# Kernel tuning notes

Hardware: AMD Instinct MI355X
Metric: run time of the kernel (lower is better)

## Reference

```python
import jax, jax.numpy as jnp
import numpy as np


def conv1x1(x, w, b):
    # x: [B,C,H,W], w: [O,C], b: [O]
    return jnp.einsum('bchw,oc->bohw', x, w) + b[None, :, None, None]


def dwconv(x, w):
    # depthwise conv, x: [B,C,H,W], w: [C,1,k,k], SAME padding (k odd, pad=k//2)
    return jax.lax.conv_general_dilated(
        x, w, window_strides=(1, 1), padding='SAME',
        dimension_numbers=('NCHW', 'OIHW', 'NCHW'),
        feature_group_count=x.shape[1])


def setup_inputs() -> dict:
    key = jax.random.key(0)
    ks = jax.random.split(key, 14)
    B, C, H, W = 16, 256, 64, 64
    OC = C // 16  # scale=16 -> 16
    WSCALE = 0.05
    r = lambda k, shape: jax.random.normal(k, shape, dtype=jnp.float32) * WSCALE
    return {
        'x': jax.random.normal(ks[0], (B, C, H, W), dtype=jnp.float32),
        'conv_w': r(ks[1], (C + 4, C)),           # 1x1 conv -> ctx (C) + gates (3+1)
        'conv_b': r(ks[2], (C + 4,)),
        'fw3': r(ks[3], (C, 1, 3, 3)),            # depthwise focal kernels
        'fw5': r(ks[4], (C, 1, 5, 5)),
        'fw7': r(ks[5], (C, 1, 7, 7)),
        'key_w': r(ks[6], (1, C)),                # Conv_key 1x1
        'key_b': r(ks[7], (1,)),
        'v1_w': r(ks[8], (OC, C)),                # Conv_value first 1x1
        'v1_b': r(ks[9], (OC,)),
        'ln_w': jnp.ones((OC,), dtype=jnp.float32),
        'ln_b': jnp.zeros((OC,), dtype=jnp.float32),
        'v2_w': r(ks[10], (C, OC)),               # Conv_value second 1x1
        'v2_b': r(ks[11], (C,)),
    }


def reference(x, conv_w, conv_b, fw3, fw5, fw7, key_w, key_b,
              v1_w, v1_b, ln_w, ln_b, v2_w, v2_b):
    B, C, H, W = x.shape
    # _contextAggregation
    t = conv1x1(x, conv_w, conv_b)          # [B, C+4, H, W]
    ctx, gates = t[:, :C], t[:, C:]         # [B,C,H,W], [B,4,H,W]
    ctx_all = jnp.zeros_like(ctx)
    for l, fw in enumerate((fw3, fw5, fw7)):
        ctx = jax.nn.gelu(dwconv(ctx, fw), approximate=False)  # torch GELU = exact erf
        ctx_all = ctx_all + ctx * gates[:, l:l + 1]
    ctx_global = jnp.mean(ctx, axis=(2, 3), keepdims=True)     # AdaptiveAvgPool2d(1)
    ctx_all = ctx_all + ctx_global * gates[:, 3:4]
    # GC-style channel attention: softmax over spatial positions
    k = conv1x1(ctx_all, key_w, key_b).reshape(B, H * W)       # [B, HW]
    k = jax.nn.softmax(k, axis=1)
    q = ctx_all.reshape(B, C, H * W)
    qk = jnp.einsum('bcn,bn->bc', q, k)[:, :, None, None]      # [B,C,1,1]
    # Conv_value: 1x1 -> LayerNorm([OC,1,1]) -> ReLU -> 1x1
    v = conv1x1(qk, v1_w, v1_b)                                # [B,OC,1,1]
    mu = jnp.mean(v, axis=(1, 2, 3), keepdims=True)
    var = jnp.var(v, axis=(1, 2, 3), keepdims=True)
    v = (v - mu) * jax.lax.rsqrt(var + 1e-5)
    v = v * ln_w[None, :, None, None] + ln_b[None, :, None, None]
    v = jax.nn.relu(v)
    v = conv1x1(v, v2_w, v2_b)                                 # [B,C,1,1]
    return ctx_all + v
```

## Files before the change

kernel.cpp:

```cpp
#include <hip/hip_runtime.h>

#define DEVFN __device__ __forceinline__

constexpr int B  = 16;
constexpr int C  = 256;
constexpr int N  = 64 * 64;
constexpr int O1 = C + 4;

typedef __attribute__((ext_vector_type(8)))  short bf16x8;
typedef __attribute__((ext_vector_type(4)))  short bf16x4;
typedef __attribute__((ext_vector_type(16))) float f32x16;
typedef __attribute__((ext_vector_type(2)))  _Float16 h2;
typedef unsigned short ushort_t;
typedef unsigned int   uint32;

DEVFN short f2bf(float f){
  union { float f; unsigned u; } p; p.f = f;
  unsigned r = p.u + 0x7fffu + ((p.u >> 16) & 1u);
  return (short)(r >> 16);
}
DEVFN unsigned pack2(float lo, float hi){
  return (unsigned)(ushort_t)f2bf(lo) | ((unsigned)(ushort_t)f2bf(hi) << 16);
}
DEVFN float lo2f(unsigned u){ union{unsigned u; float f;} p; p.u = u << 16; return p.f; }
DEVFN float hi2f(unsigned u){ union{unsigned u; float f;} p; p.u = u & 0xffff0000u; return p.f; }
DEVFN float bf2f(ushort_t s){ union{unsigned u; float f;} p; p.u = (unsigned)s << 16; return p.f; }

DEVFN float gelu_fast(float x){
  float s = x * x;
  float t = x * fmaf(s, 0.1029432f, 2.3022082f);
  float e = __builtin_amdgcn_exp2f(-t);
  return x * __builtin_amdgcn_rcpf(1.0f + e);
}

DEVFN float fdot2f(uint32 a, uint32 b, float c){
#if __has_builtin(__builtin_amdgcn_fdot2)
  return __builtin_amdgcn_fdot2(__builtin_bit_cast(h2, a),
                                __builtin_bit_cast(h2, b), c, false);
#else
  h2 ha = __builtin_bit_cast(h2, a), hb = __builtin_bit_cast(h2, b);
  return fmaf((float)ha.x, (float)hb.x, fmaf((float)ha.y, (float)hb.y, c));
#endif
}

DEVFN uint32 pkh(float a, float b){
  _Float16 ha = (_Float16)a, hb = (_Float16)b;
  return (uint32)__builtin_bit_cast(ushort_t, ha) |
         ((uint32)__builtin_bit_cast(ushort_t, hb) << 16);
}

__global__ __launch_bounds__(256)
void k_wbf(const float* __restrict__ w, ushort_t* __restrict__ wbf,
           const float* __restrict__ fw3, const float* __restrict__ fw5,
           const float* __restrict__ fw7, uint32* __restrict__ w3p,
           uint32* __restrict__ w5p, uint32* __restrict__ w7p,
           const float* __restrict__ x, ushort_t* __restrict__ xbf){
  if(blockIdx.x >= 321){
    const int blk = blockIdx.x - 321;
    const int b  = blk >> 5;
    const int kg = blk & 31;
    const float* xs = x + ((size_t)(b * 256 + kg * 8)) * N;
    ushort_t* xd = xbf + ((size_t)(b * 32 + kg)) * N * 8;
    #pragma unroll
    for(int it = 0; it < 4; it++){
      const int n = (it * 256 + threadIdx.x) * 4;
      float4 cv[8];
      #pragma unroll
      for(int j = 0; j < 8; j++) cv[j] = *(const float4*)(xs + (size_t)j * N + n);
      #pragma unroll
      for(int p = 0; p < 4; p++){
        uint4 v;
        v.x = pack2(((const float*)&cv[0])[p], ((const float*)&cv[1])[p]);
        v.y = pack2(((const float*)&cv[2])[p], ((const float*)&cv[3])[p]);
        v.z = pack2(((const float*)&cv[4])[p], ((const float*)&cv[5])[p]);
        v.w = pack2(((const float*)&cv[6])[p], ((const float*)&cv[7])[p]);
        *(uint4*)(xd + (size_t)(n + p) * 8) = v;
      }
    }
    return;
  }
  if(blockIdx.x == 320){
    const int c = threadIdx.x;
    #pragma unroll
    for(int ky = 0; ky < 3; ky++){
      const float* wr = fw3 + c * 9 + ky * 3;
      w3p[c * 6 + ky * 2 + 0] = pkh(wr[0], wr[1]);
      w3p[c * 6 + ky * 2 + 1] = pkh(wr[2], 0.f);
    }
    #pragma unroll
    for(int ky = 0; ky < 5; ky++){
      const float* wr = fw5 + c * 25 + ky * 5;
      w5p[c * 15 + ky * 3 + 0] = pkh(wr[0], wr[1]);
      w5p[c * 15 + ky * 3 + 1] = pkh(wr[2], wr[3]);
      w5p[c * 15 + ky * 3 + 2] = pkh(wr[4], 0.f);
    }
    #pragma unroll
    for(int ky = 0; ky < 7; ky++){
      const float* wr = fw7 + c * 49 + ky * 7;
      w7p[c * 28 + ky * 4 + 0] = pkh(wr[0], wr[1]);
      w7p[c * 28 + ky * 4 + 1] = pkh(wr[2], wr[3]);
      w7p[c * 28 + ky * 4 + 2] = pkh(wr[4], wr[5]);
      w7p[c * 28 + ky * 4 + 3] = pkh(wr[6], 0.f);
    }
    return;
  }
  int idx = blockIdx.x * 256 + threadIdx.x;
  int o = idx >> 8, cc = idx & 255;
  wbf[idx] = (o < O1) ? (ushort_t)f2bf(w[o * 256 + cc]) : (ushort_t)0;
}

__global__ __launch_bounds__(512, 6)
void k_conv1_mfma(const ushort_t* __restrict__ xbf, const ushort_t* __restrict__ wbf,
                  const float* __restrict__ conv_w, const float* __restrict__ bias,
                  ushort_t* __restrict__ ctxb, float* __restrict__ gates){
  __shared__ __align__(16) short wlds[8 * 256 * 8];
  __shared__ __align__(16) short xlds[2][8 * 64 * 8];
  __shared__ float sgw[4 * 256];
  __shared__ float sbias[256];
  const int tid  = threadIdx.x;
  const int wave = tid >> 6;
  const int lane = tid & 63;
  const int l31  = lane & 31;
  const int lhi  = lane >> 5;
  const int pg   = blockIdx.x;
  const int b    = pg >> 6;
  const int n0   = (pg & 63) * 64;

  #pragma unroll
  for(int i = 0; i < 2; i++) sgw[i * 512 + tid] = conv_w[256 * 256 + i * 512 + tid];
  if(tid < 256) sbias[tid] = bias[tid];
  const int gidx = tid >> 6;
  const int gn   = tid & 63;
  float gbias = (tid < 256) ? bias[256 + gidx] : 0.f;
  float gacc = 0.f;

  f32x16 acc[2];
  #pragma unroll
  for(int t = 0; t < 2; t++)
    #pragma unroll
    for(int r = 0; r < 16; r++) acc[t][r] = 0.f;

  auto glX = [&](int kc, int bf){
    const ushort_t* src = xbf + ((size_t)(b * 32 + (kc >> 3) + wave) * N + n0 + lane) * 8;
    __builtin_amdgcn_global_load_lds(
        (const __attribute__((address_space(1))) unsigned int*)src,
        (__attribute__((address_space(3))) unsigned int*)&xlds[bf][(size_t)tid * 8],
        16, 0, 0);
  };
  auto glW = [&](int kc){
    #pragma unroll
    for(int q = 0; q < 4; q++){
      const int pidx = q * 512 + tid;
      const int kg = pidx >> 8;
      const int m  = pidx & 255;
      const ushort_t* src = wbf + (size_t)m * 256 + kc + kg * 8;
      __builtin_amdgcn_global_load_lds(
          (const __attribute__((address_space(1))) unsigned int*)src,
          (__attribute__((address_space(3))) unsigned int*)&wlds[(size_t)pidx * 8],
          16, 0, 0);
    }
  };
  auto mfmaC = [&](const short* xb){
    #pragma unroll
    for(int ks = 0; ks < 4; ks++){
      const int kg = ks * 2 + lhi;
      bf16x8 af = *(const bf16x8*)&wlds[(kg * 256 + wave * 32 + l31) * 8];
      bf16x8 b0 = *(const bf16x8*)&xb[(kg * 64 + l31) * 8];
      bf16x8 b1 = *(const bf16x8*)&xb[(kg * 64 + 32 + l31) * 8];
      acc[0] = __builtin_amdgcn_mfma_f32_32x32x16_bf16(af, b0, acc[0], 0, 0, 0);
      acc[1] = __builtin_amdgcn_mfma_f32_32x32x16_bf16(af, b1, acc[1], 0, 0, 0);
    }
  };
  auto gateC = [&](const short* xb, int kc){
    if(tid < 256){
      float a = gacc;
      #pragma unroll
      for(int kg = 0; kg < 8; kg++){
        bf16x8 xv = *(const bf16x8*)&xb[(kg * 64 + gn) * 8];
        const float* gw = &sgw[gidx * 256 + kc + kg * 8];
        #pragma unroll
        for(int j = 0; j < 4; j++){
          unsigned u = ((const unsigned*)&xv)[j];
          a = fmaf(lo2f(u), gw[2 * j], a);
          a = fmaf(hi2f(u), gw[2 * j + 1], a);
        }
      }
      gacc = a;
    }
  };

  glX(0, 0); glW(0);
  __syncthreads();
  glX(64, 1);
  mfmaC(xlds[0]); gateC(xlds[0], 0);
  __syncthreads();
  glW(64);
  __syncthreads();
  glX(128, 0);
  mfmaC(xlds[1]); gateC(xlds[1], 64);
  __syncthreads();
  glW(128);
  __syncthreads();
  glX(192, 1);
  mfmaC(xlds[0]); gateC(xlds[0], 128);
  __syncthreads();
  glW(192);
  __syncthreads();
  mfmaC(xlds[1]); gateC(xlds[1], 192);

  #pragma unroll
  for(int nt = 0; nt < 2; nt++){
    const int n = n0 + nt * 32 + l31;
    #pragma unroll
    for(int r = 0; r < 16; r++){
      const int row = (r & 3) + 8 * (r >> 2) + 4 * lhi;
      const int o = wave * 32 + row;
      const float v = acc[nt][r] + sbias[o];
      _Float16 hv = (_Float16)v;
      ctxb[((size_t)(b * 256 + o)) * N + n] = __builtin_bit_cast(ushort_t, hv);
    }
  }
  if(tid < 256)
    gates[((size_t)(b * 4 + gidx)) * N + n0 + gn] = gacc + gbias;
}

constexpr int SSTR = 72;

template<int K>
DEVFN void dw_stage_dot(const short* src, const uint32* __restrict__ wp,
                        int h, int w0, float* val){
  constexpr int R = K / 2;
  constexpr int PAIRS = (K + 2) / 2;
  float acc[8];
  #pragma unroll
  for(int i = 0; i < 8; i++) acc[i] = 0.f;
  #pragma unroll
  for(int ky = 0; ky < K; ky++){
    uint32 wk[PAIRS];
    #pragma unroll
    for(int t = 0; t < PAIRS; t++) wk[t] = wp[ky * PAIRS + t];
    const int r = h + ky - R;
    if((unsigned)r < 64u){
      const short* rp = &src[r * SSTR + w0];
      uint4 a0 = *(const uint4*)rp;
      uint4 a1 = *(const uint4*)(rp + 8);
      uint32 P[8] = {a0.x, a0.y, a0.z, a0.w, a1.x, a1.y, a1.z, a1.w};
      uint32 S[7];
      #pragma unroll
      for(int j = 0; j < 7; j++)
        S[j] = __builtin_amdgcn_alignbit(P[j + 1], P[j], 16);
      #pragma unroll
      for(int i = 0; i < 8; i++){
        int j0, useP;
        if      (K == 7){ useP =  (i & 1); j0 = (i + 1) >> 1; }
        else if (K == 5){ useP = !(i & 1); j0 = (i >> 1) + 1; }
        else            { useP =  (i & 1); j0 = (i >> 1) + ((i & 1) ? 2 : 1); }
        #pragma unroll
        for(int t = 0; t < PAIRS; t++){
          const uint32 a = useP ? P[j0 + t] : S[j0 + t];
          acc[i] = fdot2f(a, wk[t], acc[i]);
        }
      }
    }
  }
  #pragma unroll
  for(int i = 0; i < 8; i++) val[i] = gelu_fast(acc[i]);
}

DEVFN void store_row_h(short* dst, int h, int w0, const float* val){
  uint32 o0 = __builtin_bit_cast(uint32, __builtin_amdgcn_cvt_pkrtz(val[0], val[1]));
  uint32 o1 = __builtin_bit_cast(uint32, __builtin_amdgcn_cvt_pkrtz(val[2], val[3]));
  uint32 o2 = __builtin_bit_cast(uint32, __builtin_amdgcn_cvt_pkrtz(val[4], val[5]));
  uint32 o3 = __builtin_bit_cast(uint32, __builtin_amdgcn_cvt_pkrtz(val[6], val[7]));
  uint2 t0; t0.x = o0; t0.y = o1;
  uint2 t1; t1.x = o2; t1.y = o3;
  *(uint2*)&dst[h * SSTR + w0 + 4] = t0;
  *(uint2*)&dst[h * SSTR + w0 + 8] = t1;
}

__global__ __launch_bounds__(512, 8)
void k_dwchain(ushort_t* __restrict__ ctxb, const uint32* __restrict__ w3p,
               const uint32* __restrict__ w5p, const uint32* __restrict__ w7p,
               const float* __restrict__ gates){
  __shared__ __align__(16) short bufA[64 * SSTR];
  __shared__ __align__(16) short bufB[64 * SSTR];
  __shared__ float wred[8];
  const int tid = threadIdx.x;
  const int plane = blockIdx.x;
  const int b = plane >> 8;
  const int c = plane & 255;
  const int h  = tid >> 3;
  const int w0 = (tid & 7) * 8;
  const int nbase = h * 64 + w0;

  if(tid < 64){
    bf16x4 z = {0, 0, 0, 0};
    *(bf16x4*)&bufA[tid * SSTR] = z;  *(bf16x4*)&bufA[tid * SSTR + 68] = z;
    *(bf16x4*)&bufB[tid * SSTR] = z;  *(bf16x4*)&bufB[tid * SSTR + 68] = z;
  }
  {
    const uint4 iv = *(const uint4*)((const short*)ctxb + (size_t)plane * N + tid * 8);
    uint2 t0; t0.x = iv.x; t0.y = iv.y;
    uint2 t1; t1.x = iv.z; t1.y = iv.w;
    *(uint2*)&bufA[h * SSTR + w0 + 4] = t0;
    *(uint2*)&bufA[h * SSTR + w0 + 8] = t1;
  }
  __syncthreads();

  float ctxp[8];
  #pragma unroll
  for(int i = 0; i < 8; i++) ctxp[i] = 0.f;
  float val[8];

  dw_stage_dot<3>(bufA, w3p + c * 6, h, w0, val);
  {
    const float* gp = gates + ((size_t)(b * 4 + 0)) * N + nbase;
    float4 ga = *(const float4*)gp, gb = *(const float4*)(gp + 4);
    ctxp[0] = fmaf(val[0], ga.x, ctxp[0]); ctxp[1] = fmaf(val[1], ga.y, ctxp[1]);
    ctxp[2] = fmaf(val[2], ga.z, ctxp[2]); ctxp[3] = fmaf(val[3], ga.w, ctxp[3]);
    ctxp[4] = fmaf(val[4], gb.x, ctxp[4]); ctxp[5] = fmaf(val[5], gb.y, ctxp[5]);
    ctxp[6] = fmaf(val[6], gb.z, ctxp[6]); ctxp[7] = fmaf(val[7], gb.w, ctxp[7]);
    store_row_h(bufB, h, w0, val);
  }
  __syncthreads();

  dw_stage_dot<5>(bufB, w5p + c * 15, h, w0, val);
  {
    const float* gp = gates + ((size_t)(b * 4 + 1)) * N + nbase;
    float4 ga = *(const float4*)gp, gb = *(const float4*)(gp + 4);
    ctxp[0] = fmaf(val[0], ga.x, ctxp[0]); ctxp[1] = fmaf(val[1], ga.y, ctxp[1]);
    ctxp[2] = fmaf(val[2], ga.z, ctxp[2]); ctxp[3] = fmaf(val[3], ga.w, ctxp[3]);
    ctxp[4] = fmaf(val[4], gb.x, ctxp[4]); ctxp[5] = fmaf(val[5], gb.y, ctxp[5]);
    ctxp[6] = fmaf(val[6], gb.z, ctxp[6]); ctxp[7] = fmaf(val[7], gb.w, ctxp[7]);
    store_row_h(bufA, h, w0, val);
  }
  __syncthreads();

  dw_stage_dot<7>(bufA, w7p + c * 28, h, w0, val);
  float lsum = 0.f;
  {
    const float* gp = gates + ((size_t)(b * 4 + 2)) * N + nbase;
    float4 ga = *(const float4*)gp, gb = *(const float4*)(gp + 4);
    ctxp[0] = fmaf(val[0], ga.x, ctxp[0]); ctxp[1] = fmaf(val[1], ga.y, ctxp[1]);
    ctxp[2] = fmaf(val[2], ga.z, ctxp[2]); ctxp[3] = fmaf(val[3], ga.w, ctxp[3]);
    ctxp[4] = fmaf(val[4], gb.x, ctxp[4]); ctxp[5] = fmaf(val[5], gb.y, ctxp[5]);
    ctxp[6] = fmaf(val[6], gb.z, ctxp[6]); ctxp[7] = fmaf(val[7], gb.w, ctxp[7]);
    #pragma unroll
    for(int i = 0; i < 8; i++) lsum += val[i];
  }
  #pragma unroll
  for(int off = 32; off > 0; off >>= 1) lsum += __shfl_xor(lsum, off, 64);
  if((tid & 63) == 0) wred[tid >> 6] = lsum;
  __syncthreads();
  float mean = 0.f;
  #pragma unroll
  for(int i = 0; i < 8; i++) mean += wred[i];
  mean *= (1.0f / 4096.0f);

  {
    const float* gp = gates + ((size_t)(b * 4 + 3)) * N + nbase;
    float4 ga = *(const float4*)gp, gb = *(const float4*)(gp + 4);
    bf16x8 ov;
    ov[0] = f2bf(fmaf(mean, ga.x, ctxp[0])); ov[1] = f2bf(fmaf(mean, ga.y, ctxp[1]));
    ov[2] = f2bf(fmaf(mean, ga.z, ctxp[2])); ov[3] = f2bf(fmaf(mean, ga.w, ctxp[3]));
    ov[4] = f2bf(fmaf(mean, gb.x, ctxp[4])); ov[5] = f2bf(fmaf(mean, gb.y, ctxp[5]));
    ov[6] = f2bf(fmaf(mean, gb.z, ctxp[6])); ov[7] = f2bf(fmaf(mean, gb.w, ctxp[7]));
    *(bf16x8*)((short*)ctxb + (size_t)plane * N + nbase) = ov;
  }
}

__global__ __launch_bounds__(256)
void k_logits(const ushort_t* __restrict__ P, const float* __restrict__ key_w,
              const float* __restrict__ key_b, float* __restrict__ logits){
  __shared__ float kw[256];
  __shared__ float part[512];
  int tid = threadIdx.x;
  kw[tid] = key_w[tid];
  __syncthreads();
  int b  = blockIdx.x >> 5;
  int n0 = (blockIdx.x & 31) * 128;
  int cpart = tid >> 6, pxp = tid & 63;
  const ushort_t* pp = P + ((size_t)(b * 256 + cpart * 64)) * N + n0 + pxp * 2;
  float a0 = 0.f, a1 = 0.f;
  #pragma unroll 8
  for(int c = 0; c < 64; c++){
    unsigned u = *(const unsigned*)(pp + (size_t)c * N);
    float kwv = kw[cpart * 64 + c];
    a0 = fmaf(lo2f(u), kwv, a0);
    a1 = fmaf(hi2f(u), kwv, a1);
  }
  part[cpart * 128 + pxp * 2]     = a0;
  part[cpart * 128 + pxp * 2 + 1] = a1;
  __syncthreads();
  if(tid < 128){
    float l = part[tid] + part[128 + tid] + part[256 + tid] + part[384 + tid];
    logits[b * N + n0 + tid] = l + key_b[0];
  }
}

__global__ __launch_bounds__(1024)
void k_softmax(float* __restrict__ kbuf){
  __shared__ float wred[16];
  int b = blockIdx.x, tid = threadIdx.x;
  const int wave = tid >> 6, lane = tid & 63;
  float v[4];
  float m = -1e30f;
  #pragma unroll
  for(int i = 0; i < 4; i++){
    v[i] = kbuf[b * N + tid + i * 1024];
    m = fmaxf(m, v[i]);
  }
  #pragma unroll
  for(int off = 32; off > 0; off >>= 1) m = fmaxf(m, __shfl_xor(m, off, 64));
  if(lane == 0) wred[wave] = m;
  __syncthreads();
  float mm = -1e30f;
  #pragma unroll
  for(int i = 0; i < 16; i++) mm = fmaxf(mm, wred[i]);
  __syncthreads();
  float s = 0.f;
  #pragma unroll
  for(int i = 0; i < 4; i++){ v[i] = __expf(v[i] - mm); s += v[i]; }
  #pragma unroll
  for(int off = 32; off > 0; off >>= 1) s += __shfl_xor(s, off, 64);
  if(lane == 0) wred[wave] = s;
  __syncthreads();
  float tot = 0.f;
  #pragma unroll
  for(int i = 0; i < 16; i++) tot += wred[i];
  float inv = 1.0f / tot;
  #pragma unroll
  for(int i = 0; i < 4; i++)
    kbuf[b * N + tid + i * 1024] = v[i] * inv;
}

__global__ __launch_bounds__(256)
void k_qk(const ushort_t* __restrict__ P, const float* __restrict__ kbuf,
          float* __restrict__ qk){
  __shared__ float red[256];
  int plane = blockIdx.x, tid = threadIdx.x;
  int b = plane >> 8;
  const unsigned* pp = (const unsigned*)(P + (size_t)plane * N);
  const float2* kp = (const float2*)(kbuf + b * N);
  float acc = 0.f;
  #pragma unroll
  for(int i = 0; i < 8; i++){
    int idx = tid + i * 256;
    unsigned u = pp[idx];
    float2 kk = kp[idx];
    acc = fmaf(lo2f(u), kk.x, acc);
    acc = fmaf(hi2f(u), kk.y, acc);
  }
  red[tid] = acc; __syncthreads();
  for(int s = 128; s > 0; s >>= 1){
    if(tid < s) red[tid] += red[tid + s];
    __syncthreads();
  }
  if(tid == 0) qk[plane] = red[0];
}

__global__ __launch_bounds__(256)
void k_v(const float* __restrict__ qk, const float* __restrict__ v1w,
         const float* __restrict__ v1b, const float* __restrict__ lnw,
         const float* __restrict__ lnb, const float* __restrict__ v2w,
         const float* __restrict__ v2b, float* __restrict__ vout){
  int b = blockIdx.x, tid = threadIdx.x;
  __shared__ float qs[256];
  __shared__ float part[256];
  __shared__ float v1s[16];
  __shared__ float vr[16];
  __shared__ float stats[2];
  qs[tid] = qk[b * 256 + tid];
  __syncthreads();
  int oc = tid >> 4, ln = tid & 15;
  float p = 0.f;
  #pragma unroll
  for(int j = 0; j < 16; j++){
    int cc = ln + j * 16;
    p = fmaf(v1w[oc * 256 + cc], qs[cc], p);
  }
  part[tid] = p;
  __syncthreads();
  if(tid < 16){
    float s = v1b[tid];
    for(int j = 0; j < 16; j++) s += part[tid * 16 + j];
    v1s[tid] = s;
  }
  __syncthreads();
  if(tid == 0){
    float mu = 0.f;
    for(int i = 0; i < 16; i++) mu += v1s[i];
    mu *= (1.f / 16.f);
    float var = 0.f;
    for(int i = 0; i < 16; i++){ float d = v1s[i] - mu; var += d * d; }
    var *= (1.f / 16.f);
    stats[0] = mu; stats[1] = rsqrtf(var + 1e-5f);
  }
  __syncthreads();
  if(tid < 16){
    float vv = (v1s[tid] - stats[0]) * stats[1] * lnw[tid] + lnb[tid];
    vr[tid] = fmaxf(vv, 0.f);
  }
  __syncthreads();
  float o = v2b[tid];
  #pragma unroll
  for(int j = 0; j < 16; j++) o = fmaf(v2w[tid * 16 + j], vr[j], o);
  vout[b * 256 + tid] = o;
}

__global__ __launch_bounds__(256)
void k_final(float* __restrict__ out, const ushort_t* __restrict__ ctxb,
             const float* __restrict__ vout){
  int idx8 = blockIdx.x * 256 + threadIdx.x;
  int plane = idx8 >> 9;
  int off = (idx8 & 511) * 8;
  bf16x8 v = *(const bf16x8*)((const short*)ctxb + (size_t)plane * N + off);
  float vv = vout[plane];
  float4 o0, o1;
  o0.x = bf2f((ushort_t)v[0]) + vv; o0.y = bf2f((ushort_t)v[1]) + vv;
  o0.z = bf2f((ushort_t)v[2]) + vv; o0.w = bf2f((ushort_t)v[3]) + vv;
  o1.x = bf2f((ushort_t)v[4]) + vv; o1.y = bf2f((ushort_t)v[5]) + vv;
  o1.z = bf2f((ushort_t)v[6]) + vv; o1.w = bf2f((ushort_t)v[7]) + vv;
  float* op = out + (size_t)plane * N + off;
  *(float4*)op = o0;
  *(float4*)(op + 4) = o1;
}

extern "C" void kernel_launch(void* const* d_in, const int* in_sizes, int n_in,
                              void* d_out, int out_size, void* d_ws, size_t ws_size,
                              hipStream_t stream){
  const float* x      = (const float*)d_in[0];
  const float* conv_w = (const float*)d_in[1];
  const float* conv_b = (const float*)d_in[2];
  const float* fw3    = (const float*)d_in[3];
  const float* fw5    = (const float*)d_in[4];
  const float* fw7    = (const float*)d_in[5];
  const float* key_w  = (const float*)d_in[6];
  const float* key_b  = (const float*)d_in[7];
  const float* v1_w   = (const float*)d_in[8];
  const float* v1_b   = (const float*)d_in[9];
  const float* ln_w   = (const float*)d_in[10];
  const float* ln_b   = (const float*)d_in[11];
  const float* v2_w   = (const float*)d_in[12];
  const float* v2_b   = (const float*)d_in[13];
  float* out = (float*)d_out;

  const size_t PL = (size_t)B * C * N;
  char* p = (char*)d_ws;
  ushort_t* ctxb = (ushort_t*)p;  p += PL * sizeof(ushort_t);
  float* gates   = (float*)p;     p += (size_t)B * 4 * N * sizeof(float);
  float* kbuf    = (float*)p;     p += (size_t)B * N * sizeof(float);
  float* qkb     = (float*)p;     p += (size_t)B * C * sizeof(float);
  float* vout    = (float*)p;     p += (size_t)B * C * sizeof(float);
  ushort_t* wbf  = (ushort_t*)p;  p += (size_t)320 * 256 * sizeof(ushort_t);
  uint32* w3p    = (uint32*)p;    p += (size_t)256 * 6 * sizeof(uint32);
  uint32* w5p    = (uint32*)p;    p += (size_t)256 * 15 * sizeof(uint32);
  uint32* w7p    = (uint32*)p;
  ushort_t* xbf  = (ushort_t*)d_out;

  k_wbf<<<833, 256, 0, stream>>>(conv_w, wbf, fw3, fw5, fw7, w3p, w5p, w7p,
                                 x, xbf);
  k_conv1_mfma<<<1024, 512, 0, stream>>>(xbf, wbf, conv_w, conv_b, ctxb, gates);
  k_dwchain<<<B * C, 512, 0, stream>>>(ctxb, w3p, w5p, w7p, gates);
  k_logits<<<512, 256, 0, stream>>>(ctxb, key_w, key_b, kbuf);
  k_softmax<<<B, 1024, 0, stream>>>(kbuf);
  k_qk<<<B * C, 256, 0, stream>>>(ctxb, kbuf, qkb);
  k_v<<<B, 256, 0, stream>>>(qkb, v1_w, v1_b, ln_w, ln_b, v2_w, v2_b, vout);
  k_final<<<8192, 256, 0, stream>>>(out, ctxb, vout);
}
```

Measured before the change: 266.8 us.

## Fuse key-logit reduction into depthwise chain via global atomics

Removes the separate k_logits kernel, which re-read the whole bf16 ctx tensor. Each k_dwchain thread now atomically adds key_w[c] times its fp32 ctx_all values into a logits buffer, and k_wbf zeroes that buffer first. key_b is dropped because softmax is invariant to a constant shift. The trade-off is about 16M float atomics, with 256 channels contending for each pixel address, plus nondeterministic summation order. The dwchain occupancy hint also drops from 8 to 6 waves.

```diff
diff --git a/kernel.cpp b/kernel.cpp
--- a/kernel.cpp
+++ b/kernel.cpp
@@ -54,7 +54,8 @@
            const float* __restrict__ fw3, const float* __restrict__ fw5,
            const float* __restrict__ fw7, uint32* __restrict__ w3p,
            uint32* __restrict__ w5p, uint32* __restrict__ w7p,
-           const float* __restrict__ x, ushort_t* __restrict__ xbf){
+           const float* __restrict__ x, ushort_t* __restrict__ xbf,
+           float* __restrict__ kbuf){
   if(blockIdx.x >= 321){
     const int blk = blockIdx.x - 321;
     const int b  = blk >> 5;
@@ -101,6 +102,11 @@
       w7p[c * 28 + ky * 4 + 1] = pkh(wr[2], wr[3]);
       w7p[c * 28 + ky * 4 + 2] = pkh(wr[4], wr[5]);
       w7p[c * 28 + ky * 4 + 3] = pkh(wr[6], 0.f);
+    }
+    float4* kz = (float4*)kbuf;
+    for(int it = 0; it < 64; it++){
+      float4 z; z.x = 0.f; z.y = 0.f; z.z = 0.f; z.w = 0.f;
+      kz[it * 256 + threadIdx.x] = z;
     }
     return;
   }
@@ -278,10 +284,11 @@
   *(uint2*)&dst[h * SSTR + w0 + 8] = t1;
 }
 
-__global__ __launch_bounds__(512, 8)
+__global__ __launch_bounds__(512, 6)
 void k_dwchain(ushort_t* __restrict__ ctxb, const uint32* __restrict__ w3p,
                const uint32* __restrict__ w5p, const uint32* __restrict__ w7p,
-               const float* __restrict__ gates){
+               const float* __restrict__ gates, const float* __restrict__ key_w,
+               float* __restrict__ kbuf){
   __shared__ __align__(16) short bufA[64 * SSTR];
   __shared__ __align__(16) short bufB[64 * SSTR];
   __shared__ float wred[8];
@@ -360,41 +367,19 @@
   {
     const float* gp = gates + ((size_t)(b * 4 + 3)) * N + nbase;
     float4 ga = *(const float4*)gp, gb = *(const float4*)(gp + 4);
+    float fv[8];
+    fv[0] = fmaf(mean, ga.x, ctxp[0]); fv[1] = fmaf(mean, ga.y, ctxp[1]);
+    fv[2] = fmaf(mean, ga.z, ctxp[2]); fv[3] = fmaf(mean, ga.w, ctxp[3]);
+    fv[4] = fmaf(mean, gb.x, ctxp[4]); fv[5] = fmaf(mean, gb.y, ctxp[5]);
+    fv[6] = fmaf(mean, gb.z, ctxp[6]); fv[7] = fmaf(mean, gb.w, ctxp[7]);
     bf16x8 ov;
-    ov[0] = f2bf(fmaf(mean, ga.x, ctxp[0])); ov[1] = f2bf(fmaf(mean, ga.y, ctxp[1]));
-    ov[2] = f2bf(fmaf(mean, ga.z, ctxp[2])); ov[3] = f2bf(fmaf(mean, ga.w, ctxp[3]));
-    ov[4] = f2bf(fmaf(mean, gb.x, ctxp[4])); ov[5] = f2bf(fmaf(mean, gb.y, ctxp[5]));
-    ov[6] = f2bf(fmaf(mean, gb.z, ctxp[6])); ov[7] = f2bf(fmaf(mean, gb.w, ctxp[7]));
+    #pragma unroll
+    for(int i = 0; i < 8; i++) ov[i] = f2bf(fv[i]);
     *(bf16x8*)((short*)ctxb + (size_t)plane * N + nbase) = ov;
-  }
-}
-
-__global__ __launch_bounds__(256)
-void k_logits(const ushort_t* __restrict__ P, const float* __restrict__ key_w,
-              const float* __restrict__ key_b, float* __restrict__ logits){
-  __shared__ float kw[256];
-  __shared__ float part[512];
-  int tid = threadIdx.x;
-  kw[tid] = key_w[tid];
-  __syncthreads();
-  int b  = blockIdx.x >> 5;
-  int n0 = (blockIdx.x & 31) * 128;
-  int cpart = tid >> 6, pxp = tid & 63;
-  const ushort_t* pp = P + ((size_t)(b * 256 + cpart * 64)) * N + n0 + pxp * 2;
-  float a0 = 0.f, a1 = 0.f;
-  #pragma unroll 8
-  for(int c = 0; c < 64; c++){
-    unsigned u = *(const unsigned*)(pp + (size_t)c * N);
-    float kwv = kw[cpart * 64 + c];
-    a0 = fmaf(lo2f(u), kwv, a0);
-    a1 = fmaf(hi2f(u), kwv, a1);
-  }
-  part[cpart * 128 + pxp * 2]     = a0;
-  part[cpart * 128 + pxp * 2 + 1] = a1;
-  __syncthreads();
-  if(tid < 128){
-    float l = part[tid] + part[128 + tid] + part[256 + tid] + part[384 + tid];
-    logits[b * N + n0 + tid] = l + key_b[0];
+    const float kwv = key_w[c];
+    float* kb = kbuf + (size_t)b * N + nbase;
+    #pragma unroll
+    for(int i = 0; i < 8; i++) atomicAdd(&kb[i], kwv * fv[i]);
   }
 }
 
@@ -544,6 +529,7 @@
   const float* v2_w   = (const float*)d_in[12];
   const float* v2_b   = (const float*)d_in[13];
   float* out = (float*)d_out;
+  (void)key_b;
 
   const size_t PL = (size_t)B * C * N;
   char* p = (char*)d_ws;
@@ -559,10 +545,9 @@
   ushort_t* xbf  = (ushort_t*)d_out;
 
   k_wbf<<<833, 256, 0, stream>>>(conv_w, wbf, fw3, fw5, fw7, w3p, w5p, w7p,
-                                 x, xbf);
+                                 x, xbf, kbuf);
   k_conv1_mfma<<<1024, 512, 0, stream>>>(xbf, wbf, conv_w, conv_b, ctxb, gates);
-  k_dwchain<<<B * C, 512, 0, stream>>>(ctxb, w3p, w5p, w7p, gates);
-  k_logits<<<512, 256, 0, stream>>>(ctxb, key_w, key_b, kbuf);
+  k_dwchain<<<B * C, 512, 0, stream>>>(ctxb, w3p, w5p, w7p, gates, key_w, kbuf);
   k_softmax<<<B, 1024, 0, stream>>>(kbuf);
   k_qk<<<B * C, 256, 0, stream>>>(ctxb, kbuf, qkb);
   k_v<<<B, 256, 0, stream>>>(qkb, v1_w, v1_b, ln_w, ln_b, v2_w, v2_b, vout);
```

New measurement: 775.7 us. 2.91x slower.

## Double-buffer weight and activation tiles in 1x1 conv MFMA with smaller K chunks

Applied to the files above, without the earlier changes.

The K-loop of the 1x1 convolution kernel is restructured from four 64-wide chunks, where the weight tile was single-buffered and reloaded between extra barriers, into eight 32-wide chunks. Both weight and activation tiles are now double-buffered, so the next chunk's loads overlap the current MFMAs with one barrier per step. This removes the serialized weight-load stalls and halves the barriers per chunk. In exchange there are more, smaller pipeline steps and only half the threads issue the X loads.

```diff
diff --git a/kernel.cpp b/kernel.cpp
--- a/kernel.cpp
+++ b/kernel.cpp
@@ -113,8 +113,8 @@
 void k_conv1_mfma(const ushort_t* __restrict__ xbf, const ushort_t* __restrict__ wbf,
                   const float* __restrict__ conv_w, const float* __restrict__ bias,
                   ushort_t* __restrict__ ctxb, float* __restrict__ gates){
-  __shared__ __align__(16) short wlds[8 * 256 * 8];
-  __shared__ __align__(16) short xlds[2][8 * 64 * 8];
+  __shared__ __align__(16) short wlds[2][4 * 256 * 8];
+  __shared__ __align__(16) short xlds[2][4 * 64 * 8];
   __shared__ float sgw[4 * 256];
   __shared__ float sbias[256];
   const int tid  = threadIdx.x;
@@ -141,42 +141,45 @@
     for(int r = 0; r < 16; r++) acc[t][r] = 0.f;
 
   auto glX = [&](int kc, int bf){
-    const ushort_t* src = xbf + ((size_t)(b * 32 + (kc >> 3) + wave) * N + n0 + lane) * 8;
-    __builtin_amdgcn_global_load_lds(
-        (const __attribute__((address_space(1))) unsigned int*)src,
-        (__attribute__((address_space(3))) unsigned int*)&xlds[bf][(size_t)tid * 8],
-        16, 0, 0);
+    if(tid < 256){
+      const int kg = tid >> 6, n = tid & 63;
+      const ushort_t* src = xbf + ((size_t)(b * 32 + (kc >> 3) + kg) * N + n0 + n) * 8;
+      __builtin_amdgcn_global_load_lds(
+          (const __attribute__((address_space(1))) unsigned int*)src,
+          (__attribute__((address_space(3))) unsigned int*)&xlds[bf][(size_t)tid * 8],
+          16, 0, 0);
+    }
   };
-  auto glW = [&](int kc){
-    #pragma unroll
-    for(int q = 0; q < 4; q++){
+  auto glW = [&](int kc, int bf){
+    #pragma unroll
+    for(int q = 0; q < 2; q++){
       const int pidx = q * 512 + tid;
       const int kg = pidx >> 8;
       const int m  = pidx & 255;
       const ushort_t* src = wbf + (size_t)m * 256 + kc + kg * 8;
       __builtin_amdgcn_global_load_lds(
           (const __attribute__((address_space(1))) unsigned int*)src,
-          (__attribute__((address_space(3))) unsigned int*)&wlds[(size_t)pidx * 8],
+          (__attribute__((address_space(3))) unsigned int*)&wlds[bf][(size_t)pidx * 8],
           16, 0, 0);
     }
   };
-  auto mfmaC = [&](const short* xb){
-    #pragma unroll
-    for(int ks = 0; ks < 4; ks++){
+  auto mfmaC = [&](int bf){
+    #pragma unroll
+    for(int ks = 0; ks < 2; ks++){
       const int kg = ks * 2 + lhi;
-      bf16x8 af = *(const bf16x8*)&wlds[(kg * 256 + wave * 32 + l31) * 8];
-      bf16x8 b0 = *(const bf16x8*)&xb[(kg * 64 + l31) * 8];
-      bf16x8 b1 = *(const bf16x8*)&xb[(kg * 64 + 32 + l31) * 8];
+      bf16x8 af = *(const bf16x8*)&wlds[bf][(kg * 256 + wave * 32 + l31) * 8];
+      bf16x8 b0 = *(const bf16x8*)&xlds[bf][(kg * 64 + l31) * 8];
+      bf16x8 b1 = *(const bf16x8*)&xlds[bf][(kg * 64 + 32 + l31) * 8];
       acc[0] = __builtin_amdgcn_mfma_f32_32x32x16_bf16(af, b0, acc[0], 0, 0, 0);
       acc[1] = __builtin_amdgcn_mfma_f32_32x32x16_bf16(af, b1, acc[1], 0, 0, 0);
     }
   };
-  auto gateC = [&](const short* xb, int kc){
+  auto gateC = [&](int bf, int kc){
     if(tid < 256){
       float a = gacc;
       #pragma unroll
-      for(int kg = 0; kg < 8; kg++){
-        bf16x8 xv = *(const bf16x8*)&xb[(kg * 64 + gn) * 8];
+      for(int kg = 0; kg < 4; kg++){
+        bf16x8 xv = *(const bf16x8*)&xlds[bf][(kg * 64 + gn) * 8];
         const float* gw = &sgw[gidx * 256 + kc + kg * 8];
         #pragma unroll
         for(int j = 0; j < 4; j++){
@@ -189,24 +192,19 @@
     }
   };
 
-  glX(0, 0); glW(0);
-  __syncthreads();
-  glX(64, 1);
-  mfmaC(xlds[0]); gateC(xlds[0], 0);
-  __syncthreads();
-  glW(64);
-  __syncthreads();
-  glX(128, 0);
-  mfmaC(xlds[1]); gateC(xlds[1], 64);
-  __syncthreads();
-  glW(128);
-  __syncthreads();
-  glX(192, 1);
-  mfmaC(xlds[0]); gateC(xlds[0], 128);
-  __syncthreads();
-  glW(192);
-  __syncthreads();
-  mfmaC(xlds[1]); gateC(xlds[1], 192);
+  glX(0, 0); glW(0, 0);
+  __syncthreads();
+  #pragma unroll
+  for(int c = 0; c < 7; c++){
+    const int bf = c & 1;
+    glX((c + 1) * 32, bf ^ 1);
+    glW((c + 1) * 32, bf ^ 1);
+    mfmaC(bf);
+    gateC(bf, c * 32);
+    __syncthreads();
+  }
+  mfmaC(1);
+  gateC(1, 224);
 
   #pragma unroll
   for(int nt = 0; nt < 2; nt++){
```

After: 263.0 us. No clear change (-1.4%).
